# Kernel optimization log

Hardware: AMD Instinct MI355X
Metric: run time of the kernel (lower is better)

## Reference

```python
import jax, jax.numpy as jnp
import numpy as np

# ---- fixed config (matches A_Sp_P4CNN cfg with n_channels=32) ----
C = 32          # n_channels
B = 32          # batch
H = W = 48      # input spatial size
KS = 3          # main conv kernel
SPK = 7         # spatial-attention kernel
EPS = 2e-5      # BatchNorm eps
NG = 4          # p4 rotation group size (n_grid)
SAME7 = [(SPK // 2, SPK // 2)] * 2  # 'same' padding for attention convs


def _conv2d(x, w, padding):
    return jax.lax.conv_general_dilated(
        x, w, window_strides=(1, 1), padding=padding,
        dimension_numbers=('NCHW', 'OIHW', 'NCHW'))


def _rot(w, r):
    # rotate kernel spatially by r*90 deg (p4 group action on Z2 kernels)
    return jnp.rot90(w, k=r, axes=(-2, -1))


def _gg_rot(w, r):
    # p4 action on a GG kernel [O,I,4,k,k]: spatial rotation + cyclic shift of
    # the input-rotation axis
    return jnp.roll(_rot(w, r), shift=r, axis=2)


def _lift_conv(x, w, padding):
    # lifting conv Z2 -> p4: x [B,Ci,H,W], w [Co,Ci,k,k] -> [B,Co,4,H',W']
    return jnp.stack([_conv2d(x, _rot(w, r), padding) for r in range(NG)], axis=2)


def _gg_conv(x, w, padding):
    # group conv p4 -> p4: x [B,Ci,4,H,W], w [Co,Ci,4,k,k] -> [B,Co,4,H',W']
    b, ci, g, h, ww = x.shape
    xf = x.reshape(b, ci * g, h, ww)
    outs = []
    for r in range(NG):
        wr = _gg_rot(w, r).reshape(w.shape[0], ci * g, w.shape[-2], w.shape[-1])
        outs.append(_conv2d(xf, wr, padding))
    return jnp.stack(outs, axis=2)


def _sp_att_rng(x, aw):
    # CBAM-style spatial attention lifted to p4: [B,Ci,H,W] -> [B,1,4,H,W]
    a = jnp.concatenate([jnp.mean(x, 1, keepdims=True),
                         jnp.max(x, 1, keepdims=True)], axis=1)
    return jax.nn.sigmoid(_lift_conv(a, aw, SAME7))


def _sp_att_gg(x, aw):
    # spatial attention on a p4 feature map: [B,Ci,4,H,W] -> [B,1,4,H,W]
    a = jnp.concatenate([jnp.mean(x, 1, keepdims=True),
                         jnp.max(x, 1, keepdims=True)], axis=1)
    return jax.nn.sigmoid(_gg_conv(a, aw, SAME7))


def _att_conv_rng(x, w, bias, aw):
    # attentive lifting conv: per output rotation r, modulate the input with the
    # r-th spatial attention map, then convolve with the r-rotated kernel
    att = _sp_att_rng(x, aw)  # [B,1,4,H,W]
    outs = [_conv2d(att[:, :, r] * x, _rot(w, r), 'VALID') for r in range(NG)]
    return jnp.stack(outs, axis=2) + bias[None, :, None, None, None]


def _att_conv_gg(x, w, bias, aw):
    # attentive group conv: attention broadcast over channels + input rotations
    att = _sp_att_gg(x, aw)  # [B,1,4,H,W]
    b, ci, g, h, ww = x.shape
    outs = []
    for r in range(NG):
        xr = (att[:, :, r][:, :, None] * x).reshape(b, ci * g, h, ww)
        wr = _gg_rot(w, r).reshape(w.shape[0], ci * g, KS, KS)
        outs.append(_conv2d(xr, wr, 'VALID'))
    return jnp.stack(outs, axis=2) + bias[None, :, None, None, None]


def _bn3d(x, gamma, beta):
    # BatchNorm3d over [B,C,4,H,W]: per-channel stats over (B,4,H,W) (training-mode math)
    m = jnp.mean(x, axis=(0, 2, 3, 4), keepdims=True)
    v = jnp.var(x, axis=(0, 2, 3, 4), keepdims=True)
    return gamma[None, :, None, None, None] * (x - m) * jax.lax.rsqrt(v + EPS) \
        + beta[None, :, None, None, None]


def _max_pool2(x):
    # max_pooling_Rn: 2x2/2 spatial max pool on [B,C,4,H,W]
    return jax.lax.reduce_window(x, -jnp.inf, jax.lax.max,
                                 (1, 1, 1, 2, 2), (1, 1, 1, 2, 2), 'VALID')


def setup_inputs() -> dict:
    key = jax.random.key(0)
    ks = jax.random.split(key, 40)
    sd = 0.1
    inp = {'x': jax.random.normal(ks[0], (B, 1, H, W), dtype=jnp.float32)}
    # c1: lifting conv 1 -> C
    inp['w1'] = jax.random.normal(ks[1], (C, 1, KS, KS), dtype=jnp.float32) * sd
    inp['b1'] = jnp.zeros((C,), jnp.float32)
    inp['aw1'] = jax.random.normal(ks[2], (1, 2, SPK, SPK), dtype=jnp.float32) * sd
    # c2..c6: GG convs C -> C
    for i in range(2, 7):
        inp[f'w{i}'] = jax.random.normal(ks[3 * i], (C, C, NG, KS, KS), dtype=jnp.float32) * sd
        inp[f'b{i}'] = jnp.zeros((C,), jnp.float32)
        inp[f'aw{i}'] = jax.random.normal(ks[3 * i + 1], (1, 2, NG, SPK, SPK), dtype=jnp.float32) * sd
    # c7: GG conv C -> 10 (classifier)
    inp['w7'] = jax.random.normal(ks[30], (10, C, NG, KS, KS), dtype=jnp.float32) * sd
    inp['b7'] = jnp.zeros((10,), jnp.float32)
    inp['aw7'] = jax.random.normal(ks[31], (1, 2, NG, SPK, SPK), dtype=jnp.float32) * sd
    # BatchNorm3d affine params bn1..bn6
    for i in range(1, 7):
        inp[f'g{i}'] = jnp.ones((C,), jnp.float32)
        inp[f'be{i}'] = jnp.zeros((C,), jnp.float32)
    return inp


def reference(x, w1, b1, aw1, w2, b2, aw2, w3, b3, aw3, w4, b4, aw4,
              w5, b5, aw5, w6, b6, aw6, w7, b7, aw7,
              g1, be1, g2, be2, g3, be3, g4, be4, g5, be5, g6, be6):
    # dropout is identity in eval-mode reference
    out = jax.nn.relu(_bn3d(_att_conv_rng(x, w1, b1, aw1), g1, be1))
    out = jax.nn.relu(_bn3d(_att_conv_gg(out, w2, b2, aw2), g2, be2))
    out = _max_pool2(out)
    out = jax.nn.relu(_bn3d(_att_conv_gg(out, w3, b3, aw3), g3, be3))
    out = jax.nn.relu(_bn3d(_att_conv_gg(out, w4, b4, aw4), g4, be4))
    out = jax.nn.relu(_bn3d(_att_conv_gg(out, w5, b5, aw5), g5, be5))
    out = jax.nn.relu(_bn3d(_att_conv_gg(out, w6, b6, aw6), g6, be6))
    out = _att_conv_gg(out, w7, b7, aw7)  # [B,10,4,h,w]
    out = jnp.max(out, axis=2)            # pool over rotation group (dim=-3)
    out = jnp.mean(out, axis=(2, 3))      # adaptive_avg_pool2d(1) + view
    return out                             # [B,10]
```

## Files before the change

kernel.cpp:

```cpp
#include <hip/hip_runtime.h>
#include <cstddef>

#define DINL static __device__ __forceinline__

typedef __attribute__((ext_vector_type(4))) float f4v;
typedef __attribute__((ext_vector_type(8))) short bh8;
typedef __attribute__((ext_vector_type(4))) unsigned short us4;

DINL void rot_src(int r, int K, int i, int j, int& si, int& sj) {
  switch (r & 3) {
    case 0:  si = i;       sj = j;       break;
    case 1:  si = j;       sj = K-1-i;   break;
    case 2:  si = K-1-i;   sj = K-1-j;   break;
    default: si = K-1-j;   sj = i;       break;
  }
}

DINL float sigmoidf(float s) { return 1.f / (1.f + __expf(-s)); }

DINL unsigned short f2bf(float f) {
  unsigned u = __builtin_bit_cast(unsigned, f);
  u += 0x7fffu + ((u >> 16) & 1u);
  return (unsigned short)(u >> 16);
}
DINL float bf2f(unsigned short h) {
  unsigned u = ((unsigned)h) << 16;
  return __builtin_bit_cast(float, u);
}

__global__ void k_prep_w(const float* __restrict__ w2, const float* __restrict__ w3,
                         const float* __restrict__ w4, const float* __restrict__ w5,
                         const float* __restrict__ w6, const float* __restrict__ w7,
                         unsigned short* __restrict__ wrot) {
  int idx = blockIdx.x * 256 + threadIdx.x;
  if (idx >= 811008) return;
  const float* w; int OM, O, base;
  if (idx < 737280) {
    int L = idx / 147456; base = L * 147456; OM = 2; O = 32;
    w = (L == 0) ? w2 : (L == 1) ? w3 : (L == 2) ? w4 : (L == 3) ? w5 : w6;
  } else { base = 737280; OM = 1; O = 10; w = w7; }
  int local = idx - base;
  int j = local & 7; int t = local >> 3;
  int lanei = t & 63; t >>= 6;
  int mi = t % OM; t /= OM;
  int ks = t & 3; t >>= 2;
  int tap = t % 9; int r = t / 9;
  int n = lanei & 15, q = lanei >> 4;
  int o = mi * 16 + n;
  int ci = q * 8 + j;
  int gs = (ks - r) & 3;
  int ky = tap / 3, kx = tap % 3;
  int si, sj; rot_src(r, 3, ky, kx, si, sj);
  float val = (o < O) ? w[((o * 32 + ci) * 4 + gs) * 9 + si * 3 + sj] : 0.f;
  wrot[idx] = f2bf(val);
}

DINL void bn_finalize_par(const float* __restrict__ partl,
                          const float* __restrict__ gamma, const float* __restrict__ beta,
                          float* st, float* l1, float* l2, int npix, int tid) {
  if (tid < 256) {
    int c = tid & 31, grp = tid >> 5;
    float s1 = 0.f, s2 = 0.f;
    #pragma unroll
    for (int k = 0; k < 8; ++k) {
      int bk = grp * 8 + k;
      s1 += partl[bk * 128 + c];
      s2 += partl[bk * 128 + 64 + c];
    }
    l1[tid] = s1; l2[tid] = s2;
  }
  __syncthreads();
  if (tid < 32) {
    float a = 0.f, q = 0.f;
    #pragma unroll
    for (int k = 0; k < 8; ++k) { a += l1[k * 32 + tid]; q += l2[k * 32 + tid]; }
    float N = 4.f * (float)npix;
    float m = a / N;
    float v = q / N - m * m;
    float inv = rsqrtf(v + 2e-5f);
    float sc = gamma[tid] * inv;
    st[tid] = sc;
    st[32 + tid] = beta[tid] - m * sc;
  }
  __syncthreads();
}

__global__ void __launch_bounds__(256)
k_att_lift(const float* __restrict__ x, const float* __restrict__ aw,
           float* __restrict__ att) {
  const int H = 48, HW = H * H;
  __shared__ float wsum[4][49];
  for (int i = threadIdx.x; i < 196; i += 256) {
    int r = i / 49; int t = i % 49;
    int ky = t / 7, kx = t % 7;
    int si, sj; rot_src(r, 7, ky, kx, si, sj);
    wsum[r][t] = aw[si * 7 + sj] + aw[49 + si * 7 + sj];
  }
  __syncthreads();
  int idx = blockIdx.x * 256 + threadIdx.x;
  if (idx >= 32 * 4 * HW) return;
  int xw = idx % H; int t = idx / H;
  int yh = t % H;  t /= H;
  int r  = t & 3;  int b = t >> 2;
  const float* xb = x + b * HW;
  float s = 0.f;
  for (int ky = 0; ky < 7; ++ky) {
    int y = yh + ky - 3;
    if ((unsigned)y >= (unsigned)H) continue;
    for (int kx = 0; kx < 7; ++kx) {
      int xx = xw + kx - 3;
      if ((unsigned)xx >= (unsigned)H) continue;
      s += xb[y * H + xx] * wsum[r][ky * 7 + kx];
    }
  }
  att[idx] = sigmoidf(s);
}

__global__ void __launch_bounds__(256)
k_conv_lift(const float* __restrict__ x, const float* __restrict__ att,
            const float* __restrict__ w, const float* __restrict__ bias,
            unsigned short* __restrict__ y, float* __restrict__ partl) {
  const int HO = 46;
  __shared__ float xs[3 * 48];
  __shared__ float as[4][3 * 48];
  __shared__ float wsm[288];
  __shared__ float bs[32];
  __shared__ float bnred[64];
  int id = blockIdx.x;
  int yo = id % HO; int b = id / HO;

  for (int i = threadIdx.x; i < 144; i += 256)
    xs[i] = x[b * 2304 + (yo + i / 48) * 48 + (i % 48)];
  for (int i = threadIdx.x; i < 576; i += 256) {
    int r = i / 144; int rem = i % 144;
    as[r][rem] = att[(b * 4 + r) * 2304 + (yo + rem / 48) * 48 + (rem % 48)];
  }
  for (int i = threadIdx.x; i < 288; i += 256) wsm[i] = w[i];
  if (threadIdx.x < 32) bs[threadIdx.x] = bias[threadIdx.x];
  if (threadIdx.x < 64) bnred[threadIdx.x] = 0.f;
  __syncthreads();

  int o = threadIdx.x & 31;
  int cl = threadIdx.x >> 5;
  float wreg[9];
  #pragma unroll
  for (int i = 0; i < 9; ++i) wreg[i] = wsm[o * 9 + i];
  float bv = bs[o];
  float sacc = 0.f, qacc = 0.f;

  for (int c8 = 0; c8 < 6; ++c8) {
    int col = c8 * 8 + cl;
    if (col < HO) {
      float xv[9];
      #pragma unroll
      for (int ky = 0; ky < 3; ++ky)
        #pragma unroll
        for (int kx = 0; kx < 3; ++kx)
          xv[ky * 3 + kx] = xs[ky * 48 + col + kx];
      unsigned short* yp = y + ((size_t)b * 2116 + yo * HO + col) * 128 + o;
      #pragma unroll
      for (int r = 0; r < 4; ++r) {
        float acc = bv;
        #pragma unroll
        for (int ky = 0; ky < 3; ++ky)
          #pragma unroll
          for (int kx = 0; kx < 3; ++kx) {
            int si, sj; rot_src(r, 3, ky, kx, si, sj);
            acc = fmaf(as[r][ky * 48 + col + kx] * xv[ky * 3 + kx], wreg[si * 3 + sj], acc);
          }
        yp[r * 32] = f2bf(acc);
        sacc += acc; qacc += acc * acc;
      }
    }
  }
  atomicAdd(&bnred[o], sacc);
  atomicAdd(&bnred[32 + o], qacc);
  __syncthreads();
  if (threadIdx.x < 64) {
    int bucket = blockIdx.x & 63;
    int c = threadIdx.x & 31;
    int off = (threadIdx.x < 32) ? c : (64 + c);
    atomicAdd(&partl[bucket * 128 + off], bnred[threadIdx.x]);
  }
}

template<int H, int OM, int O, int OSTR, bool BNS>
__global__ void __launch_bounds__(256)
k_conv_mfma(const unsigned short* __restrict__ xn, const float* __restrict__ att,
            const unsigned short* __restrict__ wl, const float* __restrict__ bias,
            unsigned short* __restrict__ y, float* __restrict__ partl) {
  constexpr int HO = H - 2, HW = H * H;
  constexpr int TR = 8, TC = 16, WR = TR + 2, WC = TC + 2, CGH = 68;
  constexpr int NRT = (HO + TR - 1) / TR, NCT = (HO + TC - 1) / TC;
  constexpr int NPIX = WR * WC;
  constexpr int NCH = NPIX * 8;
  constexpr int NST = (NCH + 255) / 256;
  __shared__ __align__(16) unsigned short xa[2][NPIX * CGH];
  __shared__ float bnred[128];

  int id = blockIdx.x;
  int slot = id & 7; int k = id >> 3;
  int tile = k % (NRT * NCT); k /= (NRT * NCT);
  int r = k & 3; int bhi = k >> 2;
  int b = bhi * 8 + slot;
  int rt = tile / NCT, ct = tile % NCT;
  int row0 = rt * TR, c0 = ct * TC;

  const unsigned short* xb = xn + (size_t)b * HW * 128;
  const float* ab = att + (size_t)(b * 4 + r) * HW;

  int tid = threadIdx.x;
  int lane = tid & 63;
  int wv = tid >> 6;
  int n = lane & 15, quad = lane >> 4;

  f4v acc[OM][2];
  #pragma unroll
  for (int mi = 0; mi < OM; ++mi)
    #pragma unroll
    for (int ri = 0; ri < 2; ++ri) {
      acc[mi][ri][0] = 0.f; acc[mi][ri][1] = 0.f;
      acc[mi][ri][2] = 0.f; acc[mi][ri][3] = 0.f;
    }

  const bh8* wa = (const bh8*)wl + (size_t)r * 9 * 4 * OM * 64 + lane;

  bh8 wqa[4], wqb[4];
  auto wload = [&](int s) {
    int hh = s / 18, tt = s % 18, tp = tt >> 1, kk = tt & 1, ks2 = hh * 2 + kk;
    wqa[s & 3] = wa[(size_t)((tp * 4 + ks2) * OM + 0) * 64];
    if constexpr (OM == 2)
      wqb[s & 3] = wa[(size_t)((tp * 4 + ks2) * OM + 1) * 64];
  };

  bh8 sx[NST]; float sa[NST];
  auto issue = [&](int half) {
    #pragma unroll
    for (int i = 0; i < NST; ++i) {
      int u = tid + i * 256;
      if (i + 1 < NST || u < NCH) {
        int ch = u & 7; int pix = u >> 3;
        int wr = pix / WC, wc = pix % WC;
        int row = row0 + wr; if (row > H - 1) row = H - 1;
        int col = c0 + wc;  if (col > H - 1) col = H - 1;
        int p = row * H + col;
        sx[i] = *(const bh8*)(xb + (size_t)p * 128 + half * 64 + ch * 8);
        sa[i] = ab[p];
      }
    }
  };
  auto wlds = [&](int half) {
    #pragma unroll
    for (int i = 0; i < NST; ++i) {
      int u = tid + i * 256;
      if (i + 1 < NST || u < NCH) {
        int ch = u & 7; int pix = u >> 3;
        bh8 v;
        #pragma unroll
        for (int j2 = 0; j2 < 8; ++j2)
          v[j2] = (short)f2bf(bf2f((unsigned short)sx[i][j2]) * sa[i]);
        *(bh8*)&xa[half][pix * CGH + ch * 8] = v;
      }
    }
  };
  auto mfma_half = [&](int half) {
    #pragma unroll
    for (int t = 0; t < 18; ++t) {
      const int s = half * 18 + t;
      bh8 a0 = wqa[s & 3];
      bh8 a1;
      if constexpr (OM == 2) a1 = wqb[s & 3];
      if (s + 4 < 36) wload(s + 4);
      const int tap = t >> 1, kl = t & 1;
      const int ky = tap / 3, kx = tap % 3;
      int pb0 = ((2 * wv + ky) * WC + n + kx) * CGH;
      int pb1 = pb0 + WC * CGH;
      bh8 b0 = *(const bh8*)&xa[half][pb0 + kl * 32 + quad * 8];
      bh8 b1 = *(const bh8*)&xa[half][pb1 + kl * 32 + quad * 8];
      acc[0][0] = __builtin_amdgcn_mfma_f32_16x16x32_bf16(a0, b0, acc[0][0], 0, 0, 0);
      acc[0][1] = __builtin_amdgcn_mfma_f32_16x16x32_bf16(a0, b1, acc[0][1], 0, 0, 0);
      if constexpr (OM == 2) {
        acc[1][0] = __builtin_amdgcn_mfma_f32_16x16x32_bf16(a1, b0, acc[1][0], 0, 0, 0);
        acc[1][1] = __builtin_amdgcn_mfma_f32_16x16x32_bf16(a1, b1, acc[1][1], 0, 0, 0);
      }
    }
  };

  wload(0); wload(1); wload(2); wload(3);
  issue(0);
  wlds(0);
  __syncthreads();
  issue(1);
  mfma_half(0);
  wlds(1);
  __syncthreads();
  mfma_half(1);

  float sv[OM * 4], qv[OM * 4];
  #pragma unroll
  for (int e = 0; e < OM * 4; ++e) { sv[e] = 0.f; qv[e] = 0.f; }
  #pragma unroll
  for (int mi = 0; mi < OM; ++mi)
    #pragma unroll
    for (int ri = 0; ri < 2; ++ri) {
      int prow = row0 + 2 * wv + ri;
      int col = c0 + n;
      if (prow < HO && col < HO) {
        unsigned short* yp = y + ((size_t)b * HO * HO + prow * HO + col) * OSTR;
        int o0 = mi * 16 + quad * 4;
        f4v v = acc[mi][ri];
        if constexpr (O == 32) {
          us4 w4;
          #pragma unroll
          for (int reg = 0; reg < 4; ++reg) {
            float val = v[reg] + bias[o0 + reg];
            w4[reg] = f2bf(val);
            if constexpr (BNS) { sv[mi * 4 + reg] += val; qv[mi * 4 + reg] += val * val; }
          }
          *(us4*)(yp + r * 32 + o0) = w4;
        } else {
          #pragma unroll
          for (int reg = 0; reg < 4; ++reg) {
            int o = o0 + reg;
            if (o < O) yp[r * O + o] = f2bf(v[reg] + bias[o]);
          }
        }
      }
    }

  if constexpr (BNS) {
    #pragma unroll
    for (int e = 0; e < OM * 4; ++e) {
      #pragma unroll
      for (int off = 1; off < 16; off <<= 1) {
        sv[e] += __shfl_xor(sv[e], off);
        qv[e] += __shfl_xor(qv[e], off);
      }
    }
    if (threadIdx.x < 128) bnred[threadIdx.x] = 0.f;
    __syncthreads();
    if (n == 0) {
      #pragma unroll
      for (int e = 0; e < OM * 4; ++e) {
        int o = (e >> 2) * 16 + quad * 4 + (e & 3);
        atomicAdd(&bnred[o], sv[e]);
        atomicAdd(&bnred[64 + o], qv[e]);
      }
    }
    __syncthreads();
    if (threadIdx.x < 128)
      atomicAdd(&partl[(blockIdx.x & 63) * 128 + threadIdx.x], bnred[threadIdx.x]);
  }
}

__global__ void __launch_bounds__(256)
k_meanmax_bn(const unsigned short* __restrict__ yr, const float* __restrict__ partl,
             const float* __restrict__ gamma, const float* __restrict__ beta,
             unsigned short* __restrict__ xn, unsigned short* __restrict__ amap,
             int npix) {
  __shared__ float st[64];
  __shared__ float l1[256], l2[256];
  bn_finalize_par(partl, gamma, beta, st, l1, l2, npix, threadIdx.x);
  int idx = blockIdx.x * 256 + threadIdx.x;
  if (idx >= npix) return;
  const unsigned short* yp = yr + (size_t)idx * 128;
  unsigned short* xp = xn + (size_t)idx * 128;
  float sm[4] = {0.f, 0.f, 0.f, 0.f};
  float mx[4] = {-1e30f, -1e30f, -1e30f, -1e30f};
  #pragma unroll 4
  for (int oo = 0; oo < 16; ++oo) {
    int g = oo >> 2, ob = (oo & 3) * 8;
    bh8 raw = *(const bh8*)(yp + oo * 8);
    bh8 w;
    #pragma unroll
    for (int e = 0; e < 8; ++e) {
      float v = fmaxf(fmaf(bf2f((unsigned short)raw[e]), st[ob + e], st[32 + ob + e]), 0.f);
      w[e] = (short)f2bf(v);
      sm[g] += v;
      mx[g] = fmaxf(mx[g], v);
    }
    *(bh8*)(xp + oo * 8) = w;
  }
  bh8 am;
  #pragma unroll
  for (int g = 0; g < 4; ++g) {
    am[g] = (short)f2bf(sm[g] * (1.f / 32.f));
    am[4 + g] = (short)f2bf(mx[g]);
  }
  *(bh8*)(amap + (size_t)idx * 8) = am;
}

template<int HIN, int HOUT, bool POOL>
__global__ void __launch_bounds__(256)
k_postA(const unsigned short* __restrict__ yr, const float* __restrict__ partl,
        const float* __restrict__ gamma, const float* __restrict__ beta,
        unsigned short* __restrict__ xn, unsigned short* __restrict__ amap) {
  __shared__ float st[64];
  __shared__ float l1[256], l2[256];
  bn_finalize_par(partl, gamma, beta, st, l1, l2, 32 * HIN * HIN, threadIdx.x);
  int idx = blockIdx.x * 256 + threadIdx.x;
  if (idx >= 32 * HOUT * HOUT * 4) return;
  int g = idx & 3; int p = idx >> 2;
  int col = p % HOUT; int t = p / HOUT;
  int row = t % HOUT; int b = t / HOUT;
  float sm = 0.f, mx = -1e30f;
  unsigned short* xp = xn + (size_t)p * 128 + g * 32;
  if constexpr (POOL) {
    const unsigned short* p00 =
        yr + ((size_t)b * HIN * HIN + (row * 2) * HIN + col * 2) * 128 + g * 32;
    #pragma unroll
    for (int k = 0; k < 4; ++k) {
      bh8 r0 = *(const bh8*)(p00 + k * 8);
      bh8 r1 = *(const bh8*)(p00 + 128 + k * 8);
      bh8 r2 = *(const bh8*)(p00 + (size_t)HIN * 128 + k * 8);
      bh8 r3 = *(const bh8*)(p00 + (size_t)(HIN + 1) * 128 + k * 8);
      bh8 w;
      #pragma unroll
      for (int e = 0; e < 8; ++e) {
        float sc = st[k * 8 + e], sh = st[32 + k * 8 + e];
        float a0 = fmaxf(fmaf(bf2f((unsigned short)r0[e]), sc, sh), 0.f);
        float a1 = fmaxf(fmaf(bf2f((unsigned short)r1[e]), sc, sh), 0.f);
        float a2 = fmaxf(fmaf(bf2f((unsigned short)r2[e]), sc, sh), 0.f);
        float a3 = fmaxf(fmaf(bf2f((unsigned short)r3[e]), sc, sh), 0.f);
        float val = fmaxf(fmaxf(a0, a1), fmaxf(a2, a3));
        w[e] = (short)f2bf(val);
        sm += val; mx = fmaxf(mx, val);
      }
      *(bh8*)(xp + k * 8) = w;
    }
  } else {
    const unsigned short* yp = yr + (size_t)p * 128 + g * 32;
    #pragma unroll
    for (int k = 0; k < 4; ++k) {
      bh8 raw = *(const bh8*)(yp + k * 8);
      bh8 w;
      #pragma unroll
      for (int e = 0; e < 8; ++e) {
        float v = fmaxf(fmaf(bf2f((unsigned short)raw[e]), st[k * 8 + e], st[32 + k * 8 + e]), 0.f);
        w[e] = (short)f2bf(v);
        sm += v;
        mx = fmaxf(mx, v);
      }
      *(bh8*)(xp + k * 8) = w;
    }
  }
  amap[(size_t)p * 8 + g] = f2bf(sm * (1.f / 32.f));
  amap[(size_t)p * 8 + 4 + g] = f2bf(mx);
}

__global__ void __launch_bounds__(256)
k_att_gg(const unsigned short* __restrict__ amap, const float* __restrict__ aw,
         float* __restrict__ att, int h) {
  __shared__ float wsa[4][4][49], wsx[4][4][49];
  for (int i = threadIdx.x; i < 784; i += 256) {
    int r = i / 196; int rem = i % 196;
    int g = rem / 49; int t = rem % 49;
    int ky = t / 7, kx = t % 7;
    int si, sj; rot_src(r, 7, ky, kx, si, sj);
    int gs = (g - r) & 3;
    wsa[r][g][t] = aw[gs * 49 + si * 7 + sj];
    wsx[r][g][t] = aw[(4 + gs) * 49 + si * 7 + sj];
  }
  __syncthreads();
  int hw = h * h;
  int idx = blockIdx.x * 256 + threadIdx.x;
  if (idx >= 32 * 4 * hw) return;
  int p = idx % hw; int t = idx / hw;
  int r = t & 3; int b = t >> 2;
  int yh = p / h, xw = p % h;
  float s = 0.f;
  for (int ky = 0; ky < 7; ++ky) {
    int y = yh + ky - 3;
    if ((unsigned)y >= (unsigned)h) continue;
    for (int kx = 0; kx < 7; ++kx) {
      int xx = xw + kx - 3;
      if ((unsigned)xx >= (unsigned)h) continue;
      int tp = ky * 7 + kx;
      bh8 av = *(const bh8*)(amap + ((size_t)b * hw + y * h + xx) * 8);
      #pragma unroll
      for (int g = 0; g < 4; ++g)
        s += bf2f((unsigned short)av[g]) * wsa[r][g][tp]
           + bf2f((unsigned short)av[4 + g]) * wsx[r][g][tp];
    }
  }
  att[idx] = sigmoidf(s);
}

__global__ void k_final(const unsigned short* __restrict__ y7, float* __restrict__ out) {
  int idx = blockIdx.x * blockDim.x + threadIdx.x;
  if (idx >= 320) return;
  int o = idx % 10; int b = idx / 10;
  const unsigned short* p = y7 + (size_t)b * 144 * 40;
  float s = 0.f;
  for (int sp = 0; sp < 144; ++sp) {
    const unsigned short* q = p + sp * 40 + o;
    float m = fmaxf(fmaxf(bf2f(q[0]), bf2f(q[10])), fmaxf(bf2f(q[20]), bf2f(q[30])));
    s += m;
  }
  out[idx] = s * (1.f / 144.f);
}


extern "C" void kernel_launch(void* const* d_in, const int* in_sizes, int n_in,
                              void* d_out, int out_size, void* d_ws, size_t ws_size,
                              hipStream_t stream) {
  (void)in_sizes; (void)n_in; (void)out_size; (void)ws_size;
  const float* x   = (const float*)d_in[0];
  const float* w1  = (const float*)d_in[1];
  const float* b1  = (const float*)d_in[2];
  const float* aw1 = (const float*)d_in[3];
  const float* W[6];  const float* BI[6]; const float* AW[6];
  for (int i = 0; i < 6; ++i) {
    W[i]  = (const float*)d_in[4 + 3 * i];
    BI[i] = (const float*)d_in[5 + 3 * i];
    AW[i] = (const float*)d_in[6 + 3 * i];
  }
  const float* G[6]; const float* BE[6];
  for (int i = 0; i < 6; ++i) {
    G[i]  = (const float*)d_in[22 + 2 * i];
    BE[i] = (const float*)d_in[23 + 2 * i];
  }
  float* out = (float*)d_out;

  float* ws = (float*)d_ws;
  unsigned short* YR = (unsigned short*)ws;
  unsigned short* XN = (unsigned short*)(ws + 4333568);
  unsigned short* AMAP = (unsigned short*)(ws + 8667136);
  float* ATT = ws + 8937984;
  unsigned short* WROT = (unsigned short*)(ws + 9232896);
  float* PART  = ws + 9638400;

  auto cdiv = [](int a, int b) { return (a + b - 1) / b; };
  float* PL[6];
  for (int i = 0; i < 6; ++i) PL[i] = PART + i * 8192;

  hipMemsetAsync(PART, 0, 6 * 8192 * sizeof(float), stream);

  k_prep_w<<<dim3(cdiv(811008, 256)), dim3(256), 0, stream>>>(
      W[0], W[1], W[2], W[3], W[4], W[5], WROT);
  const unsigned short* WL[6];
  for (int i = 0; i < 5; ++i) WL[i] = WROT + i * 147456;
  WL[5] = WROT + 737280;

  {
    int natt = 32 * 4 * 48 * 48;
    k_att_lift<<<dim3(cdiv(natt, 256)), dim3(256), 0, stream>>>(x, aw1, ATT);
    k_conv_lift<<<dim3(32 * 46), dim3(256), 0, stream>>>(x, ATT, w1, b1, YR, PL[0]);
    int npix = 32 * 2116;
    k_meanmax_bn<<<dim3(cdiv(npix, 256)), dim3(256), 0, stream>>>(YR, PL[0], G[0], BE[0], XN, AMAP, npix);
    k_att_gg<<<dim3(cdiv(npix * 4, 256)), dim3(256), 0, stream>>>(AMAP, AW[0], ATT, 46);
  }
  k_conv_mfma<46, 2, 32, 128, true><<<dim3(128 * 6 * 3), dim3(256), 0, stream>>>(XN, ATT, WL[0], BI[0], YR, PL[1]);
  k_postA<44, 22, true><<<dim3(cdiv(32 * 22 * 22 * 4, 256)), dim3(256), 0, stream>>>(YR, PL[1], G[1], BE[1], XN, AMAP);
  k_att_gg<<<dim3(cdiv(32 * 4 * 22 * 22, 256)), dim3(256), 0, stream>>>(AMAP, AW[1], ATT, 22);
  k_conv_mfma<22, 2, 32, 128, true><<<dim3(128 * 3 * 2), dim3(256), 0, stream>>>(XN, ATT, WL[1], BI[1], YR, PL[2]);
  k_postA<20, 20, false><<<dim3(cdiv(32 * 20 * 20 * 4, 256)), dim3(256), 0, stream>>>(YR, PL[2], G[2], BE[2], XN, AMAP);
  k_att_gg<<<dim3(cdiv(32 * 4 * 20 * 20, 256)), dim3(256), 0, stream>>>(AMAP, AW[2], ATT, 20);
  k_conv_mfma<20, 2, 32, 128, true><<<dim3(128 * 3 * 2), dim3(256), 0, stream>>>(XN, ATT, WL[2], BI[2], YR, PL[3]);
  k_postA<18, 18, false><<<dim3(cdiv(32 * 18 * 18 * 4, 256)), dim3(256), 0, stream>>>(YR, PL[3], G[3], BE[3], XN, AMAP);
  k_att_gg<<<dim3(cdiv(32 * 4 * 18 * 18, 256)), dim3(256), 0, stream>>>(AMAP, AW[3], ATT, 18);
  k_conv_mfma<18, 2, 32, 128, true><<<dim3(128 * 2 * 1), dim3(256), 0, stream>>>(XN, ATT, WL[3], BI[3], YR, PL[4]);
  k_postA<16, 16, false><<<dim3(cdiv(32 * 16 * 16 * 4, 256)), dim3(256), 0, stream>>>(YR, PL[4], G[4], BE[4], XN, AMAP);
  k_att_gg<<<dim3(cdiv(32 * 4 * 16 * 16, 256)), dim3(256), 0, stream>>>(AMAP, AW[4], ATT, 16);
  k_conv_mfma<16, 2, 32, 128, true><<<dim3(128 * 2 * 1), dim3(256), 0, stream>>>(XN, ATT, WL[4], BI[4], YR, PL[5]);
  k_postA<14, 14, false><<<dim3(cdiv(32 * 14 * 14 * 4, 256)), dim3(256), 0, stream>>>(YR, PL[5], G[5], BE[5], XN, AMAP);
  k_att_gg<<<dim3(cdiv(32 * 4 * 14 * 14, 256)), dim3(256), 0, stream>>>(AMAP, AW[5], ATT, 14);
  k_conv_mfma<14, 1, 10, 40, false><<<dim3(128 * 2 * 1), dim3(256), 0, stream>>>(XN, ATT, WL[5], BI[5], YR, nullptr);
  k_final<<<dim3(5), dim3(64), 0, stream>>>(YR, out);
}
```

Before: 408.0 us.

## Fuse BN/ReLU/mean-max with spatial attention conv per row band; merge prep kernels

Merges the weight prep, the first attention-lift conv and the partial-sum zeroing into a single launch, which replaces the memset and two kernels. Fuses the post-conv BN+ReLU(+pool) kernel with the 7x7 spatial-attention conv. Each block handles a band of rows for one batch image and keeps the mean/max map in shared memory with a 3-row halo, so the global amap round trip and one launch per layer go away. In exchange, the halo rows are recomputed by neighbouring bands, and the grid becomes much smaller (128 to 256 blocks), which may underfill the GPU.

```diff
diff --git a/kernel.cpp b/kernel.cpp
--- a/kernel.cpp
+++ b/kernel.cpp
@@ -26,33 +26,6 @@
 DINL float bf2f(unsigned short h) {
   unsigned u = ((unsigned)h) << 16;
   return __builtin_bit_cast(float, u);
-}
-
-__global__ void k_prep_w(const float* __restrict__ w2, const float* __restrict__ w3,
-                         const float* __restrict__ w4, const float* __restrict__ w5,
-                         const float* __restrict__ w6, const float* __restrict__ w7,
-                         unsigned short* __restrict__ wrot) {
-  int idx = blockIdx.x * 256 + threadIdx.x;
-  if (idx >= 811008) return;
-  const float* w; int OM, O, base;
-  if (idx < 737280) {
-    int L = idx / 147456; base = L * 147456; OM = 2; O = 32;
-    w = (L == 0) ? w2 : (L == 1) ? w3 : (L == 2) ? w4 : (L == 3) ? w5 : w6;
-  } else { base = 737280; OM = 1; O = 10; w = w7; }
-  int local = idx - base;
-  int j = local & 7; int t = local >> 3;
-  int lanei = t & 63; t >>= 6;
-  int mi = t % OM; t /= OM;
-  int ks = t & 3; t >>= 2;
-  int tap = t % 9; int r = t / 9;
-  int n = lanei & 15, q = lanei >> 4;
-  int o = mi * 16 + n;
-  int ci = q * 8 + j;
-  int gs = (ks - r) & 3;
-  int ky = tap / 3, kx = tap % 3;
-  int si, sj; rot_src(r, 3, ky, kx, si, sj);
-  float val = (o < O) ? w[((o * 32 + ci) * 4 + gs) * 9 + si * 3 + sj] : 0.f;
-  wrot[idx] = f2bf(val);
 }
 
 DINL void bn_finalize_par(const float* __restrict__ partl,
@@ -86,34 +59,75 @@
 }
 
 __global__ void __launch_bounds__(256)
-k_att_lift(const float* __restrict__ x, const float* __restrict__ aw,
-           float* __restrict__ att) {
-  const int H = 48, HW = H * H;
+k_prep_att(const float* __restrict__ w2, const float* __restrict__ w3,
+           const float* __restrict__ w4, const float* __restrict__ w5,
+           const float* __restrict__ w6, const float* __restrict__ w7,
+           unsigned short* __restrict__ wrot,
+           const float* __restrict__ x, const float* __restrict__ aw1,
+           float* __restrict__ att, float* __restrict__ part) {
   __shared__ float wsum[4][49];
-  for (int i = threadIdx.x; i < 196; i += 256) {
-    int r = i / 49; int t = i % 49;
-    int ky = t / 7, kx = t % 7;
-    int si, sj; rot_src(r, 7, ky, kx, si, sj);
-    wsum[r][t] = aw[si * 7 + sj] + aw[49 + si * 7 + sj];
-  }
-  __syncthreads();
-  int idx = blockIdx.x * 256 + threadIdx.x;
-  if (idx >= 32 * 4 * HW) return;
-  int xw = idx % H; int t = idx / H;
-  int yh = t % H;  t /= H;
-  int r  = t & 3;  int b = t >> 2;
-  const float* xb = x + b * HW;
-  float s = 0.f;
-  for (int ky = 0; ky < 7; ++ky) {
-    int y = yh + ky - 3;
-    if ((unsigned)y >= (unsigned)H) continue;
-    for (int kx = 0; kx < 7; ++kx) {
-      int xx = xw + kx - 3;
-      if ((unsigned)xx >= (unsigned)H) continue;
-      s += xb[y * H + xx] * wsum[r][ky * 7 + kx];
-    }
-  }
-  att[idx] = sigmoidf(s);
+  __shared__ float xs[12 * 48];
+  int bid = blockIdx.x;
+  if (bid < 3168) {
+    int idx = bid * 256 + threadIdx.x;
+    const float* w; int OM, O, base;
+    if (idx < 737280) {
+      int L = idx / 147456; base = L * 147456; OM = 2; O = 32;
+      w = (L == 0) ? w2 : (L == 1) ? w3 : (L == 2) ? w4 : (L == 3) ? w5 : w6;
+    } else { base = 737280; OM = 1; O = 10; w = w7; }
+    int local = idx - base;
+    int j = local & 7; int t = local >> 3;
+    int lanei = t & 63; t >>= 6;
+    int mi = t % OM; t /= OM;
+    int ks = t & 3; t >>= 2;
+    int tap = t % 9; int r = t / 9;
+    int n = lanei & 15, q = lanei >> 4;
+    int o = mi * 16 + n;
+    int ci = q * 8 + j;
+    int gs = (ks - r) & 3;
+    int ky = tap / 3, kx = tap % 3;
+    int si, sj; rot_src(r, 3, ky, kx, si, sj);
+    float val = (o < O) ? w[((o * 32 + ci) * 4 + gs) * 9 + si * 3 + sj] : 0.f;
+    wrot[idx] = f2bf(val);
+  } else if (bid < 4192) {
+    const int H = 48, HW = H * H, BH = 6, NB = 8;
+    int id = bid - 3168;
+    int band = id % NB; int t = id / NB;
+    int r = t & 3; int b = t >> 2;
+    int row0 = band * BH;
+    int base = row0 - 3;
+    for (int i = threadIdx.x; i < 196; i += 256) {
+      int rr = i / 49; int tt = i % 49;
+      int ky = tt / 7, kx = tt % 7;
+      int si, sj; rot_src(rr, 7, ky, kx, si, sj);
+      wsum[rr][tt] = aw1[si * 7 + sj] + aw1[49 + si * 7 + sj];
+    }
+    const float* xb = x + b * HW;
+    for (int i = threadIdx.x; i < 12 * 48; i += 256) {
+      int rr = base + i / 48;
+      xs[i] = ((unsigned)rr < (unsigned)H) ? xb[rr * H + (i % 48)] : 0.f;
+    }
+    __syncthreads();
+    for (int i = threadIdx.x; i < BH * H; i += 256) {
+      int yh = row0 + i / H; int xw = i % H;
+      float s = 0.f;
+      for (int ky = 0; ky < 7; ++ky) {
+        int y = yh + ky - 3;
+        if ((unsigned)y >= (unsigned)H) continue;
+        for (int kx = 0; kx < 7; ++kx) {
+          int xx = xw + kx - 3;
+          if ((unsigned)xx >= (unsigned)H) continue;
+          s += xs[(y - base) * H + xx] * wsum[r][ky * 7 + kx];
+        }
+      }
+      att[(size_t)(b * 4 + r) * HW + yh * H + xw] = sigmoidf(s);
+    }
+  } else {
+    int zb = bid - 4192;
+    int off = zb * 2048 + threadIdx.x;
+    #pragma unroll
+    for (int k = 0; k < 8; ++k) part[off + k * 256] = 0.f;
+  }
 }
 
 __global__ void __launch_bounds__(256)
@@ -353,106 +367,27 @@
   }
 }
 
+template<int HIN, int HOUT, bool POOL, int BH, int NB>
 __global__ void __launch_bounds__(256)
-k_meanmax_bn(const unsigned short* __restrict__ yr, const float* __restrict__ partl,
-             const float* __restrict__ gamma, const float* __restrict__ beta,
-             unsigned short* __restrict__ xn, unsigned short* __restrict__ amap,
-             int npix) {
+k_postB(const unsigned short* __restrict__ yr, const float* __restrict__ partl,
+        const float* __restrict__ gamma, const float* __restrict__ beta,
+        const float* __restrict__ aw,
+        unsigned short* __restrict__ xn, float* __restrict__ att) {
+  constexpr int AR = BH + 6;
+  __shared__ float wsa[4][4][49], wsx[4][4][49];
   __shared__ float st[64];
   __shared__ float l1[256], l2[256];
-  bn_finalize_par(partl, gamma, beta, st, l1, l2, npix, threadIdx.x);
-  int idx = blockIdx.x * 256 + threadIdx.x;
-  if (idx >= npix) return;
-  const unsigned short* yp = yr + (size_t)idx * 128;
-  unsigned short* xp = xn + (size_t)idx * 128;
-  float sm[4] = {0.f, 0.f, 0.f, 0.f};
-  float mx[4] = {-1e30f, -1e30f, -1e30f, -1e30f};
-  #pragma unroll 4
-  for (int oo = 0; oo < 16; ++oo) {
-    int g = oo >> 2, ob = (oo & 3) * 8;
-    bh8 raw = *(const bh8*)(yp + oo * 8);
-    bh8 w;
-    #pragma unroll
-    for (int e = 0; e < 8; ++e) {
-      float v = fmaxf(fmaf(bf2f((unsigned short)raw[e]), st[ob + e], st[32 + ob + e]), 0.f);
-      w[e] = (short)f2bf(v);
-      sm[g] += v;
-      mx[g] = fmaxf(mx[g], v);
-    }
-    *(bh8*)(xp + oo * 8) = w;
-  }
-  bh8 am;
-  #pragma unroll
-  for (int g = 0; g < 4; ++g) {
-    am[g] = (short)f2bf(sm[g] * (1.f / 32.f));
-    am[4 + g] = (short)f2bf(mx[g]);
-  }
-  *(bh8*)(amap + (size_t)idx * 8) = am;
-}
-
-template<int HIN, int HOUT, bool POOL>
-__global__ void __launch_bounds__(256)
-k_postA(const unsigned short* __restrict__ yr, const float* __restrict__ partl,
-        const float* __restrict__ gamma, const float* __restrict__ beta,
-        unsigned short* __restrict__ xn, unsigned short* __restrict__ amap) {
-  __shared__ float st[64];
-  __shared__ float l1[256], l2[256];
-  bn_finalize_par(partl, gamma, beta, st, l1, l2, 32 * HIN * HIN, threadIdx.x);
-  int idx = blockIdx.x * 256 + threadIdx.x;
-  if (idx >= 32 * HOUT * HOUT * 4) return;
-  int g = idx & 3; int p = idx >> 2;
-  int col = p % HOUT; int t = p / HOUT;
-  int row = t % HOUT; int b = t / HOUT;
-  float sm = 0.f, mx = -1e30f;
-  unsigned short* xp = xn + (size_t)p * 128 + g * 32;
-  if constexpr (POOL) {
-    const unsigned short* p00 =
-        yr + ((size_t)b * HIN * HIN + (row * 2) * HIN + col * 2) * 128 + g * 32;
-    #pragma unroll
-    for (int k = 0; k < 4; ++k) {
-      bh8 r0 = *(const bh8*)(p00 + k * 8);
-      bh8 r1 = *(const bh8*)(p00 + 128 + k * 8);
-      bh8 r2 = *(const bh8*)(p00 + (size_t)HIN * 128 + k * 8);
-      bh8 r3 = *(const bh8*)(p00 + (size_t)(HIN + 1) * 128 + k * 8);
-      bh8 w;
-      #pragma unroll
-      for (int e = 0; e < 8; ++e) {
-        float sc = st[k * 8 + e], sh = st[32 + k * 8 + e];
-        float a0 = fmaxf(fmaf(bf2f((unsigned short)r0[e]), sc, sh), 0.f);
-        float a1 = fmaxf(fmaf(bf2f((unsigned short)r1[e]), sc, sh), 0.f);
-        float a2 = fmaxf(fmaf(bf2f((unsigned short)r2[e]), sc, sh), 0.f);
-        float a3 = fmaxf(fmaf(bf2f((unsigned short)r3[e]), sc, sh), 0.f);
-        float val = fmaxf(fmaxf(a0, a1), fmaxf(a2, a3));
-        w[e] = (short)f2bf(val);
-        sm += val; mx = fmaxf(mx, val);
-      }
-      *(bh8*)(xp + k * 8) = w;
-    }
-  } else {
-    const unsigned short* yp = yr + (size_t)p * 128 + g * 32;
-    #pragma unroll
-    for (int k = 0; k < 4; ++k) {
-      bh8 raw = *(const bh8*)(yp + k * 8);
-      bh8 w;
-      #pragma unroll
-      for (int e = 0; e < 8; ++e) {
-        float v = fmaxf(fmaf(bf2f((unsigned short)raw[e]), st[k * 8 + e], st[32 + k * 8 + e]), 0.f);
-        w[e] = (short)f2bf(v);
-        sm += v;
-        mx = fmaxf(mx, v);
-      }
-      *(bh8*)(xp + k * 8) = w;
-    }
-  }
-  amap[(size_t)p * 8 + g] = f2bf(sm * (1.f / 32.f));
-  amap[(size_t)p * 8 + 4 + g] = f2bf(mx);
-}
-
-__global__ void __launch_bounds__(256)
-k_att_gg(const unsigned short* __restrict__ amap, const float* __restrict__ aw,
-         float* __restrict__ att, int h) {
-  __shared__ float wsa[4][4][49], wsx[4][4][49];
-  for (int i = threadIdx.x; i < 784; i += 256) {
+  __shared__ __align__(16) unsigned short amap_l[AR * HOUT * 8];
+  int tid = threadIdx.x;
+  int band = blockIdx.x % NB;
+  int b = blockIdx.x / NB;
+  int row0 = band * BH;
+  int row1 = row0 + BH; if (row1 > HOUT) row1 = HOUT;
+  int lo = row0 - 3; if (lo < 0) lo = 0;
+  int hi = row1 + 3; if (hi > HOUT) hi = HOUT;
+  int base = row0 - 3;
+
+  for (int i = tid; i < 784; i += 256) {
     int r = i / 196; int rem = i % 196;
     int g = rem / 49; int t = rem % 49;
     int ky = t / 7, kx = t % 7;
@@ -461,29 +396,90 @@
     wsa[r][g][t] = aw[gs * 49 + si * 7 + sj];
     wsx[r][g][t] = aw[(4 + gs) * 49 + si * 7 + sj];
   }
-  __syncthreads();
-  int hw = h * h;
-  int idx = blockIdx.x * 256 + threadIdx.x;
-  if (idx >= 32 * 4 * hw) return;
-  int p = idx % hw; int t = idx / hw;
-  int r = t & 3; int b = t >> 2;
-  int yh = p / h, xw = p % h;
-  float s = 0.f;
-  for (int ky = 0; ky < 7; ++ky) {
-    int y = yh + ky - 3;
-    if ((unsigned)y >= (unsigned)h) continue;
-    for (int kx = 0; kx < 7; ++kx) {
-      int xx = xw + kx - 3;
-      if ((unsigned)xx >= (unsigned)h) continue;
-      int tp = ky * 7 + kx;
-      bh8 av = *(const bh8*)(amap + ((size_t)b * hw + y * h + xx) * 8);
-      #pragma unroll
-      for (int g = 0; g < 4; ++g)
-        s += bf2f((unsigned short)av[g]) * wsa[r][g][tp]
-           + bf2f((unsigned short)av[4 + g]) * wsx[r][g][tp];
-    }
-  }
-  att[idx] = sigmoidf(s);
+  bn_finalize_par(partl, gamma, beta, st, l1, l2, 32 * HIN * HIN, tid);
+
+  int npx = (hi - lo) * HOUT;
+  for (int i = tid; i < npx; i += 256) {
+    int row = lo + i / HOUT, col = i % HOUT;
+    int p = row * HOUT + col;
+    bool owned = (row >= row0 && row < row1);
+    float sm[4] = {0.f, 0.f, 0.f, 0.f};
+    float mx[4] = {-1e30f, -1e30f, -1e30f, -1e30f};
+    unsigned short* xp = xn + ((size_t)b * HOUT * HOUT + p) * 128;
+    if constexpr (POOL) {
+      int y0 = row * 2, x0 = col * 2;
+      const unsigned short* p00 = yr + ((size_t)b * HIN * HIN + y0 * HIN + x0) * 128;
+      #pragma unroll 2
+      for (int oo = 0; oo < 16; ++oo) {
+        int g = oo >> 2, ob = (oo & 3) * 8;
+        bh8 r0 = *(const bh8*)(p00 + oo * 8);
+        bh8 r1 = *(const bh8*)(p00 + 128 + oo * 8);
+        bh8 r2 = *(const bh8*)(p00 + (size_t)HIN * 128 + oo * 8);
+        bh8 r3 = *(const bh8*)(p00 + (size_t)(HIN + 1) * 128 + oo * 8);
+        bh8 w;
+        #pragma unroll
+        for (int e = 0; e < 8; ++e) {
+          float sc = st[ob + e], sh = st[32 + ob + e];
+          float a0 = fmaxf(fmaf(bf2f((unsigned short)r0[e]), sc, sh), 0.f);
+          float a1 = fmaxf(fmaf(bf2f((unsigned short)r1[e]), sc, sh), 0.f);
+          float a2 = fmaxf(fmaf(bf2f((unsigned short)r2[e]), sc, sh), 0.f);
+          float a3 = fmaxf(fmaf(bf2f((unsigned short)r3[e]), sc, sh), 0.f);
+          float val = fmaxf(fmaxf(a0, a1), fmaxf(a2, a3));
+          w[e] = (short)f2bf(val);
+          sm[g] += val; mx[g] = fmaxf(mx[g], val);
+        }
+        if (owned) *(bh8*)(xp + oo * 8) = w;
+      }
+    } else {
+      const unsigned short* yp = yr + ((size_t)b * HIN * HIN + p) * 128;
+      #pragma unroll 4
+      for (int oo = 0; oo < 16; ++oo) {
+        int g = oo >> 2, ob = (oo & 3) * 8;
+        bh8 raw = *(const bh8*)(yp + oo * 8);
+        bh8 w;
+        #pragma unroll
+        for (int e = 0; e < 8; ++e) {
+          float v = fmaxf(fmaf(bf2f((unsigned short)raw[e]), st[ob + e], st[32 + ob + e]), 0.f);
+          w[e] = (short)f2bf(v);
+          sm[g] += v;
+          mx[g] = fmaxf(mx[g], v);
+        }
+        if (owned) *(bh8*)(xp + oo * 8) = w;
+      }
+    }
+    bh8 am;
+    #pragma unroll
+    for (int g = 0; g < 4; ++g) {
+      am[g] = (short)f2bf(sm[g] * (1.f / 32.f));
+      am[4 + g] = (short)f2bf(mx[g]);
+    }
+    *(bh8*)&amap_l[((row - base) * HOUT + col) * 8] = am;
+  }
+  __syncthreads();
+
+  int nrow = row1 - row0;
+  int nout = 4 * nrow * HOUT;
+  for (int i = tid; i < nout; i += 256) {
+    int r = i / (nrow * HOUT);
+    int rem = i % (nrow * HOUT);
+    int yh = row0 + rem / HOUT, xw = rem % HOUT;
+    float s = 0.f;
+    for (int ky = 0; ky < 7; ++ky) {
+      int y = yh + ky - 3;
+      if ((unsigned)y >= (unsigned)HOUT) continue;
+      for (int kx = 0; kx < 7; ++kx) {
+        int xx = xw + kx - 3;
+        if ((unsigned)xx >= (unsigned)HOUT) continue;
+        int tp = ky * 7 + kx;
+        bh8 av = *(const bh8*)&amap_l[((y - base) * HOUT + xx) * 8];
+        #pragma unroll
+        for (int g = 0; g < 4; ++g)
+          s += bf2f((unsigned short)av[g]) * wsa[r][g][tp]
+             + bf2f((unsigned short)av[4 + g]) * wsx[r][g][tp];
+      }
+    }
+    att[((size_t)(b * 4 + r)) * HOUT * HOUT + yh * HOUT + xw] = sigmoidf(s);
+  }
 }
 
 __global__ void k_final(const unsigned short* __restrict__ y7, float* __restrict__ out) {
@@ -525,46 +521,31 @@
   float* ws = (float*)d_ws;
   unsigned short* YR = (unsigned short*)ws;
   unsigned short* XN = (unsigned short*)(ws + 4333568);
-  unsigned short* AMAP = (unsigned short*)(ws + 8667136);
   float* ATT = ws + 8937984;
   unsigned short* WROT = (unsigned short*)(ws + 9232896);
   float* PART  = ws + 9638400;
 
-  auto cdiv = [](int a, int b) { return (a + b - 1) / b; };
   float* PL[6];
   for (int i = 0; i < 6; ++i) PL[i] = PART + i * 8192;
 
-  hipMemsetAsync(PART, 0, 6 * 8192 * sizeof(float), stream);
-
-  k_prep_w<<<dim3(cdiv(811008, 256)), dim3(256), 0, stream>>>(
-      W[0], W[1], W[2], W[3], W[4], W[5], WROT);
+  k_prep_att<<<dim3(4216), dim3(256), 0, stream>>>(
+      W[0], W[1], W[2], W[3], W[4], W[5], WROT, x, aw1, ATT, PART);
   const unsigned short* WL[6];
   for (int i = 0; i < 5; ++i) WL[i] = WROT + i * 147456;
   WL[5] = WROT + 737280;
 
-  {
-    int natt = 32 * 4 * 48 * 48;
-    k_att_lift<<<dim3(cdiv(natt, 256)), dim3(256), 0, stream>>>(x, aw1, ATT);
-    k_conv_lift<<<dim3(32 * 46), dim3(256), 0, stream>>>(x, ATT, w1, b1, YR, PL[0]);
-    int npix = 32 * 2116;
-    k_meanmax_bn<<<dim3(cdiv(npix, 256)), dim3(256), 0, stream>>>(YR, PL[0], G[0], BE[0], XN, AMAP, npix);
-    k_att_gg<<<dim3(cdiv(npix * 4, 256)), dim3(256), 0, stream>>>(AMAP, AW[0], ATT, 46);
-  }
+  k_conv_lift<<<dim3(32 * 46), dim3(256), 0, stream>>>(x, ATT, w1, b1, YR, PL[0]);
+  k_postB<46, 46, false, 6, 8><<<dim3(32 * 8), dim3(256), 0, stream>>>(YR, PL[0], G[0], BE[0], AW[0], XN, ATT);
   k_conv_mfma<46, 2, 32, 128, true><<<dim3(128 * 6 * 3), dim3(256), 0, stream>>>(XN, ATT, WL[0], BI[0], YR, PL[1]);
-  k_postA<44, 22, true><<<dim3(cdiv(32 * 22 * 22 * 4, 256)), dim3(256), 0, stream>>>(YR, PL[1], G[1], BE[1], XN, AMAP);
-  k_att_gg<<<dim3(cdiv(32 * 4 * 22 * 22, 256)), dim3(256), 0, stream>>>(AMAP, AW[1], ATT, 22);
+  k_postB<44, 22, true, 6, 4><<<dim3(32 * 4), dim3(256), 0, stream>>>(YR, PL[1], G[1], BE[1], AW[1], XN, ATT);
   k_conv_mfma<22, 2, 32, 128, true><<<dim3(128 * 3 * 2), dim3(256), 0, stream>>>(XN, ATT, WL[1], BI[1], YR, PL[2]);
-  k_postA<20, 20, false><<<dim3(cdiv(32 * 20 * 20 * 4, 256)), dim3(256), 0, stream>>>(YR, PL[2], G[2], BE[2], XN, AMAP);
-  k_att_gg<<<dim3(cdiv(32 * 4 * 20 * 20, 256)), dim3(256), 0, stream>>>(AMAP, AW[2], ATT, 20);
+  k_postB<20, 20, false, 5, 4><<<dim3(32 * 4), dim3(256), 0, stream>>>(YR, PL[2], G[2], BE[2], AW[2], XN, ATT);
   k_conv_mfma<20, 2, 32, 128, true><<<dim3(128 * 3 * 2), dim3(256), 0, stream>>>(XN, ATT, WL[2], BI[2], YR, PL[3]);
-  k_postA<18, 18, false><<<dim3(cdiv(32 * 18 * 18 * 4, 256)), dim3(256), 0, stream>>>(YR, PL[3], G[3], BE[3], XN, AMAP);
-  k_att_gg<<<dim3(cdiv(32 * 4 * 18 * 18, 256)), dim3(256), 0, stream>>>(AMAP, AW[3], ATT, 18);
+  k_postB<18, 18, false, 5, 4><<<dim3(32 * 4), dim3(256), 0, stream>>>(YR, PL[3], G[3], BE[3], AW[3], XN, ATT);
   k_conv_mfma<18, 2, 32, 128, true><<<dim3(128 * 2 * 1), dim3(256), 0, stream>>>(XN, ATT, WL[3], BI[3], YR, PL[4]);
-  k_postA<16, 16, false><<<dim3(cdiv(32 * 16 * 16 * 4, 256)), dim3(256), 0, stream>>>(YR, PL[4], G[4], BE[4], XN, AMAP);
-  k_att_gg<<<dim3(cdiv(32 * 4 * 16 * 16, 256)), dim3(256), 0, stream>>>(AMAP, AW[4], ATT, 16);
+  k_postB<16, 16, false, 4, 4><<<dim3(32 * 4), dim3(256), 0, stream>>>(YR, PL[4], G[4], BE[4], AW[4], XN, ATT);
   k_conv_mfma<16, 2, 32, 128, true><<<dim3(128 * 2 * 1), dim3(256), 0, stream>>>(XN, ATT, WL[4], BI[4], YR, PL[5]);
-  k_postA<14, 14, false><<<dim3(cdiv(32 * 14 * 14 * 4, 256)), dim3(256), 0, stream>>>(YR, PL[5], G[5], BE[5], XN, AMAP);
-  k_att_gg<<<dim3(cdiv(32 * 4 * 14 * 14, 256)), dim3(256), 0, stream>>>(AMAP, AW[5], ATT, 14);
+  k_postB<14, 14, false, 4, 4><<<dim3(32 * 4), dim3(256), 0, stream>>>(YR, PL[5], G[5], BE[5], AW[5], XN, ATT);
   k_conv_mfma<14, 1, 10, 40, false><<<dim3(128 * 2 * 1), dim3(256), 0, stream>>>(XN, ATT, WL[5], BI[5], YR, nullptr);
   k_final<<<dim3(5), dim3(64), 0, stream>>>(YR, out);
 }
```

Result: slower. 555.4 us (+36.1%).
